# Optimization experiments

Measured on AMD Instinct MI355X. Metric: run time of the kernel, lower is better.

The kernel has to match this reference:

```python
import jax, jax.numpy as jnp
import numpy as np

B, T, E, K, D = 8, 4096, 1024, 128, 1024


def setup_inputs() -> dict:
    key = jax.random.key(0)
    ks = jax.random.split(key, 5)
    scale_w = 1.0 / np.sqrt(E)
    x = jax.random.normal(ks[0], (B, T, E), dtype=jnp.float32)
    mu = jax.random.normal(ks[1], (1, K, E), dtype=jnp.float32) * scale_w
    bias = jax.random.normal(ks[2], (1, K), dtype=jnp.float32) * scale_w
    Wr = jax.random.normal(ks[3], (D, K * E), dtype=jnp.float32) * (1.0 / np.sqrt(K * E))
    Wl = jax.random.normal(ks[4], (K * E, D), dtype=jnp.float32) * (1.0 / np.sqrt(D))
    k = jnp.float32(1.0)
    b = jnp.float32(0.0)
    return {"x": x, "mu": mu, "bias": bias, "Wr": Wr, "Wl": Wl, "k": k, "b": b}


def reference(x, mu, bias, Wr, Wl, k, b):
    # x: [B,T,E], mu: [1,K,E]
    inv_sqrt_E = 1.0 / jnp.sqrt(jnp.float32(E))
    # att = mu @ x^T / sqrt(E) -> [B,K,T]
    att = jnp.einsum('ke,bte->bkt', mu[0], x) * inv_sqrt_E
    part = jax.nn.logsumexp(att, axis=-1)            # [B,K]
    attp = jax.nn.softmax(att, axis=-1)              # [B,K,T]
    sel = jnp.einsum('bkt,bte->bke', attp, x)        # [B,K,E]
    # lre*sel + (1-lre)*sel is mathematically identity; preserved from source
    lre = jax.nn.sigmoid(part - bias)[:, :, None]
    sel = lre * sel + (1.0 - lre) * sel
    # low-rank MLP (dsel is computed but unused in the original forward)
    xr = jax.nn.relu(sel.reshape(x.shape[0], -1) @ Wr.T)   # [B,D]
    dsel = (xr @ Wl.T).reshape(sel.shape)                   # [B,K,E] (unused)
    # attention-transpose combine + residual + affine
    dx = jnp.einsum('bkt,bke->bte', attp, sel)              # [B,T,E]
    out = k * (x + dx) + b
    return out
```

## Files before the change

kernel.cpp:

```cpp
#include <hip/hip_runtime.h>

#define B_ 8
#define T_ 4096
#define E_ 1024
#define K_ 128

typedef __bf16 bf16;
typedef bf16 bf16x8 __attribute__((ext_vector_type(8)));
typedef bf16 bf16x4 __attribute__((ext_vector_type(4)));
typedef float f32x4 __attribute__((ext_vector_type(4)));

__global__ __launch_bounds__(256) void k0_cvt_mu(const float* __restrict__ mu,
                                                 bf16* __restrict__ mub) {
    int i = blockIdx.x * 256 + threadIdx.x;
    mub[i] = (bf16)mu[i];
}

__global__ __launch_bounds__(256) void k1_att(const float* __restrict__ x,
                                              const bf16* __restrict__ mub,
                                              bf16* __restrict__ attPh,
                                              bf16* __restrict__ xb) {
    const int b = blockIdx.z;
    const int h = blockIdx.y;
    const int t0 = blockIdx.x * 64;
    const int tid = threadIdx.x;
    const int w = tid >> 6, lane = tid & 63, g = lane >> 4, ln = lane & 15;

    __shared__ bf16 xs[64][72];
    __shared__ bf16 ms[128][72];

    f32x4 acc[8];
#pragma unroll
    for (int m = 0; m < 8; ++m) acc[m] = (f32x4){0.f, 0.f, 0.f, 0.f};

    const int rx = tid >> 4, cx = (tid & 15) * 4;
    const int rm = tid >> 3, cm = (tid & 7) * 8;

    for (int c = 0; c < 8; ++c) {
        const int ebase = h * 512 + c * 64;
#pragma unroll
        for (int p = 0; p < 4; ++p) {
            const int row = p * 16 + rx;
            f32x4 v = *(const f32x4*)(x + ((size_t)(b * T_ + t0 + row)) * E_ + ebase + cx);
            bf16x4 o;
            o[0] = (bf16)v[0]; o[1] = (bf16)v[1]; o[2] = (bf16)v[2]; o[3] = (bf16)v[3];
            *(bf16x4*)&xs[row][cx] = o;
            *(bf16x4*)(xb + ((size_t)(b * T_ + t0 + row)) * E_ + ebase + cx) = o;
        }
#pragma unroll
        for (int p = 0; p < 4; ++p) {
            const int row = p * 32 + rm;
            *(bf16x8*)&ms[row][cm] =
                *(const bf16x8*)(mub + (size_t)row * E_ + ebase + cm);
        }
        __syncthreads();
#pragma unroll
        for (int s = 0; s < 2; ++s) {
            const int es = s * 32 + g * 8;
            bf16x8 bf = *(const bf16x8*)&xs[w * 16 + ln][es];
#pragma unroll
            for (int m = 0; m < 8; ++m) {
                bf16x8 af = *(const bf16x8*)&ms[m * 16 + ln][es];
                acc[m] = __builtin_amdgcn_mfma_f32_16x16x32_bf16(af, bf, acc[m], 0, 0, 0);
            }
        }
        __syncthreads();
    }
    const int t = t0 + w * 16 + ln;
#pragma unroll
    for (int m = 0; m < 8; ++m)
#pragma unroll
        for (int r = 0; r < 4; ++r)
            attPh[(((size_t)h * B_ + b) * K_ + m * 16 + g * 4 + r) * T_ + t] =
                (bf16)acc[m][r];
}

__global__ __launch_bounds__(256) void k2_softmax(const bf16* __restrict__ attPh,
                                                  bf16* __restrict__ attp) {
    const int row = blockIdx.x;
    const int tid = threadIdx.x;
    const bf16* p0 = attPh + (size_t)row * T_;
    const bf16* p1 = attPh + (size_t)(B_ * K_) * T_ + (size_t)row * T_;
    float v[16];
    float m = -1e30f;
#pragma unroll
    for (int i = 0; i < 2; ++i) {
        const int off = (i * 256 + tid) * 8;
        bf16x8 a = *(const bf16x8*)(p0 + off);
        bf16x8 c = *(const bf16x8*)(p1 + off);
#pragma unroll
        for (int j = 0; j < 8; ++j) {
            const float val = ((float)a[j] + (float)c[j]) * 0.03125f;
            v[i * 8 + j] = val;
            m = fmaxf(m, val);
        }
    }
#pragma unroll
    for (int off = 32; off > 0; off >>= 1) m = fmaxf(m, __shfl_xor(m, off));
    __shared__ float redm[4], reds[4];
    const int wave = tid >> 6, lane = tid & 63;
    if (lane == 0) redm[wave] = m;
    __syncthreads();
    m = fmaxf(fmaxf(redm[0], redm[1]), fmaxf(redm[2], redm[3]));
    float s = 0.f;
#pragma unroll
    for (int i = 0; i < 16; ++i) {
        v[i] = __expf(v[i] - m);
        s += v[i];
    }
#pragma unroll
    for (int off = 32; off > 0; off >>= 1) s += __shfl_xor(s, off);
    if (lane == 0) reds[wave] = s;
    __syncthreads();
    const float inv = 1.f / (reds[0] + reds[1] + reds[2] + reds[3]);
#pragma unroll
    for (int i = 0; i < 2; ++i) {
        const int off = (i * 256 + tid) * 8;
        bf16x8 o;
#pragma unroll
        for (int j = 0; j < 8; ++j) o[j] = (bf16)(v[i * 8 + j] * inv);
        *(bf16x8*)(attp + (size_t)row * T_ + off) = o;
    }
}

__global__ __launch_bounds__(256) void k4_sel(const bf16* __restrict__ xb,
                                              const bf16* __restrict__ attp,
                                              bf16* __restrict__ selpT) {
    const int e0 = blockIdx.x * 64;
    const int chunk = blockIdx.y;
    const int b = blockIdx.z;
    const int tid = threadIdx.x;
    const int w = tid >> 6, lane = tid & 63, g = lane >> 4, ln = lane & 15;

    __shared__ __align__(16) char smem[27648];
    bf16 (*as_)[72] = (bf16(*)[72])smem;
    bf16 (*xs2)[72] = (bf16(*)[72])(smem + 18432);

    f32x4 acc[8];
#pragma unroll
    for (int m = 0; m < 8; ++m) acc[m] = (f32x4){0.f, 0.f, 0.f, 0.f};

    const int rs = tid >> 3, cs = (tid & 7) * 8;

    for (int sub = 0; sub < 8; ++sub) {
        const int tc = chunk * 512 + sub * 64;
#pragma unroll
        for (int p = 0; p < 4; ++p) {
            const int row = p * 32 + rs;
            *(bf16x8*)&as_[row][cs] =
                *(const bf16x8*)(attp + ((size_t)(b * K_ + row)) * T_ + tc + cs);
        }
#pragma unroll
        for (int p = 0; p < 2; ++p) {
            const int row = p * 32 + rs;
            *(bf16x8*)&xs2[row][cs] =
                *(const bf16x8*)(xb + ((size_t)(b * T_ + tc + row)) * E_ + e0 + cs);
        }
        __syncthreads();
#pragma unroll
        for (int s = 0; s < 2; ++s) {
            const int ts = s * 32 + g * 8;
            bf16x8 bf;
#pragma unroll
            for (int j = 0; j < 8; ++j) bf[j] = xs2[ts + j][w * 16 + ln];
#pragma unroll
            for (int m = 0; m < 8; ++m) {
                bf16x8 af = *(const bf16x8*)&as_[m * 16 + ln][ts];
                acc[m] = __builtin_amdgcn_mfma_f32_16x16x32_bf16(af, bf, acc[m], 0, 0, 0);
            }
        }
        __syncthreads();
    }
    bf16 (*tlb)[136] = (bf16(*)[136])smem;
#pragma unroll
    for (int m = 0; m < 8; ++m)
#pragma unroll
        for (int r = 0; r < 4; ++r)
            tlb[w * 16 + ln][m * 16 + g * 4 + r] = (bf16)acc[m][r];
    __syncthreads();
    bf16* dst = selpT + ((size_t)chunk * B_ + b) * E_ * K_ + (size_t)e0 * K_;
#pragma unroll
    for (int rr = 0; rr < 4; ++rr) {
        const int slot = rr * 256 + tid;
        const int ee = slot >> 4;
        const int kq = slot & 15;
        bf16x8 o = *(bf16x8*)&tlb[ee][kq * 8];
        *(bf16x8*)(dst + (size_t)ee * K_ + kq * 8) = o;
    }
}

__global__ __launch_bounds__(256) void k4b_reduce(const bf16* __restrict__ selpT,
                                                  bf16* __restrict__ selbT) {
    const size_t gid = (size_t)blockIdx.x * 256 + threadIdx.x;
    const size_t f = gid * 8;
    float s[8];
#pragma unroll
    for (int j = 0; j < 8; ++j) s[j] = 0.f;
#pragma unroll
    for (int c = 0; c < 8; ++c) {
        bf16x8 v = *(const bf16x8*)(selpT + (size_t)c * (B_ * E_ * K_) + f);
#pragma unroll
        for (int j = 0; j < 8; ++j) s[j] += (float)v[j];
    }
    bf16x8 o;
#pragma unroll
    for (int j = 0; j < 8; ++j) o[j] = (bf16)s[j];
    *(bf16x8*)(selbT + f) = o;
}

__global__ __launch_bounds__(256) void k5_out(const bf16* __restrict__ xb,
                                              const bf16* __restrict__ attp,
                                              const bf16* __restrict__ selbT,
                                              const float* __restrict__ kp,
                                              const float* __restrict__ bp,
                                              float* __restrict__ out) {
    const int b = blockIdx.z;
    const int t0 = blockIdx.x * 64;
    const int e0 = blockIdx.y * 64;
    const int tid = threadIdx.x;
    const int w = tid >> 6, lane = tid & 63, g = lane >> 4, ln = lane & 15;
    const float kk = kp[0], bb = bp[0];
    __shared__ bf16 pT[64][128];
    __shared__ bf16 sb[64][136];

    {
        const int u = tid & 3;
        const int kr = tid >> 2;
#pragma unroll
        for (int p = 0; p < 2; ++p) {
            const int k = p * 64 + kr;
            const bf16* src = attp + ((size_t)b * K_ + k) * T_ + t0 + u * 16;
#pragma unroll
            for (int hh = 0; hh < 2; ++hh) {
                bf16x8 v = *(const bf16x8*)(src + hh * 8);
#pragma unroll
                for (int j = 0; j < 8; ++j) {
                    const int t = u * 16 + hh * 8 + j;
                    pT[t][k ^ (j << 3)] = v[j];
                }
            }
        }
    }
    {
        const int er = tid >> 2;
        const int kc = (tid & 3) * 32;
        const bf16* src = selbT + ((size_t)b * E_ + e0 + er) * K_ + kc;
#pragma unroll
        for (int q = 0; q < 4; ++q)
            *(bf16x8*)&sb[er][kc + q * 8] = *(const bf16x8*)(src + q * 8);
    }
    __syncthreads();

    const int tl = w * 16 + ln;
    f32x4 acc[4];
#pragma unroll
    for (int m = 0; m < 4; ++m) acc[m] = (f32x4){0.f, 0.f, 0.f, 0.f};

#pragma unroll
    for (int ks = 0; ks < 4; ++ks) {
        const int k0 = ks * 32 + g * 8;
        bf16x8 bfr = *(const bf16x8*)&pT[tl][k0 ^ ((tl & 7) << 3)];
#pragma unroll
        for (int m = 0; m < 4; ++m) {
            bf16x8 af = *(const bf16x8*)&sb[m * 16 + ln][k0];
            acc[m] = __builtin_amdgcn_mfma_f32_16x16x32_bf16(af, bfr, acc[m], 0, 0, 0);
        }
    }

    const int t = t0 + tl;
#pragma unroll
    for (int m = 0; m < 4; ++m) {
        const int e = e0 + m * 16 + g * 4;
        const size_t idx = ((size_t)b * T_ + t) * E_ + e;
        bf16x4 xv = *(const bf16x4*)(xb + idx);
        f32x4 o;
        o[0] = kk * ((float)xv[0] + acc[m][0]) + bb;
        o[1] = kk * ((float)xv[1] + acc[m][1]) + bb;
        o[2] = kk * ((float)xv[2] + acc[m][2]) + bb;
        o[3] = kk * ((float)xv[3] + acc[m][3]) + bb;
        *(f32x4*)(out + idx) = o;
    }
}

extern "C" void kernel_launch(void* const* d_in, const int* in_sizes, int n_in,
                              void* d_out, int out_size, void* d_ws, size_t ws_size,
                              hipStream_t stream) {
    const float* x  = (const float*)d_in[0];
    const float* mu = (const float*)d_in[1];
    const float* kp = (const float*)d_in[5];
    const float* bp = (const float*)d_in[6];
    float* out = (float*)d_out;

    char* ws = (char*)d_ws;
    bf16*  attPh = (bf16*)(ws);
    bf16*  selpT = (bf16*)(ws);
    bf16*  attp  = (bf16*)(ws + 16777216);
    bf16*  selbT = (bf16*)(ws + 25165824);
    bf16*  mub   = (bf16*)(ws + 27262976);
    bf16*  xb    = (bf16*)(ws + 27525120);

    k0_cvt_mu<<<dim3(512), 256, 0, stream>>>(mu, mub);
    k1_att<<<dim3(64, 2, 8), 256, 0, stream>>>(x, mub, attPh, xb);
    k2_softmax<<<dim3(1024), 256, 0, stream>>>(attPh, attp);
    k4_sel<<<dim3(16, 8, 8), 256, 0, stream>>>(xb, attp, selpT);
    k4b_reduce<<<dim3(512), 256, 0, stream>>>(selpT, selbT);
    k5_out<<<dim3(64, 16, 8), 256, 0, stream>>>(xb, attp, selbT, kp, bp, out);
}
```

Baseline: 135.1 us.

## Pre-transpose attention probabilities and read MFMA operands directly from global

```diff
diff --git a/kernel.cpp b/kernel.cpp
--- a/kernel.cpp
+++ b/kernel.cpp
@@ -123,6 +123,28 @@
     }
 }
 
+__global__ __launch_bounds__(256) void k3_transpose(const bf16* __restrict__ attp,
+                                                    bf16* __restrict__ attpT) {
+    const int b = blockIdx.y;
+    const int t0 = blockIdx.x * 64;
+    const int tid = threadIdx.x;
+    __shared__ bf16 tile[128][66];
+    const int kk = tid >> 1, half = tid & 1;
+#pragma unroll
+    for (int q = 0; q < 4; ++q)
+        *(bf16x8*)&tile[kk][half * 32 + q * 8] =
+            *(const bf16x8*)(attp + ((size_t)b * K_ + kk) * T_ + t0 + half * 32 + q * 8);
+    __syncthreads();
+    const int tt = tid & 63, kslot = (tid >> 6) * 32;
+#pragma unroll
+    for (int q = 0; q < 4; ++q) {
+        bf16x8 o;
+#pragma unroll
+        for (int j = 0; j < 8; ++j) o[j] = tile[kslot + q * 8 + j][tt];
+        *(bf16x8*)(attpT + ((size_t)b * T_ + t0 + tt) * K_ + kslot + q * 8) = o;
+    }
+}
+
 __global__ __launch_bounds__(256) void k4_sel(const bf16* __restrict__ xb,
                                               const bf16* __restrict__ attp,
                                               bf16* __restrict__ selpT) {
@@ -209,7 +231,7 @@
 }
 
 __global__ __launch_bounds__(256) void k5_out(const bf16* __restrict__ xb,
-                                              const bf16* __restrict__ attp,
+                                              const bf16* __restrict__ attpT,
                                               const bf16* __restrict__ selbT,
                                               const float* __restrict__ kp,
                                               const float* __restrict__ bp,
@@ -220,49 +242,21 @@
     const int tid = threadIdx.x;
     const int w = tid >> 6, lane = tid & 63, g = lane >> 4, ln = lane & 15;
     const float kk = kp[0], bb = bp[0];
-    __shared__ bf16 pT[64][128];
-    __shared__ bf16 sb[64][136];
-
-    {
-        const int u = tid & 3;
-        const int kr = tid >> 2;
-#pragma unroll
-        for (int p = 0; p < 2; ++p) {
-            const int k = p * 64 + kr;
-            const bf16* src = attp + ((size_t)b * K_ + k) * T_ + t0 + u * 16;
-#pragma unroll
-            for (int hh = 0; hh < 2; ++hh) {
-                bf16x8 v = *(const bf16x8*)(src + hh * 8);
-#pragma unroll
-                for (int j = 0; j < 8; ++j) {
-                    const int t = u * 16 + hh * 8 + j;
-                    pT[t][k ^ (j << 3)] = v[j];
-                }
-            }
-        }
-    }
-    {
-        const int er = tid >> 2;
-        const int kc = (tid & 3) * 32;
-        const bf16* src = selbT + ((size_t)b * E_ + e0 + er) * K_ + kc;
-#pragma unroll
-        for (int q = 0; q < 4; ++q)
-            *(bf16x8*)&sb[er][kc + q * 8] = *(const bf16x8*)(src + q * 8);
-    }
-    __syncthreads();
 
     const int tl = w * 16 + ln;
     f32x4 acc[4];
 #pragma unroll
     for (int m = 0; m < 4; ++m) acc[m] = (f32x4){0.f, 0.f, 0.f, 0.f};
 
+    const bf16* brow = attpT + ((size_t)b * T_ + t0 + tl) * K_;
+    const bf16* arow = selbT + ((size_t)b * E_ + e0 + ln) * K_;
 #pragma unroll
     for (int ks = 0; ks < 4; ++ks) {
         const int k0 = ks * 32 + g * 8;
-        bf16x8 bfr = *(const bf16x8*)&pT[tl][k0 ^ ((tl & 7) << 3)];
+        bf16x8 bfr = *(const bf16x8*)(brow + k0);
 #pragma unroll
         for (int m = 0; m < 4; ++m) {
-            bf16x8 af = *(const bf16x8*)&sb[m * 16 + ln][k0];
+            bf16x8 af = *(const bf16x8*)(arow + (size_t)(m * 16) * K_ + k0);
             acc[m] = __builtin_amdgcn_mfma_f32_16x16x32_bf16(af, bfr, acc[m], 0, 0, 0);
         }
     }
@@ -298,11 +292,13 @@
     bf16*  selbT = (bf16*)(ws + 25165824);
     bf16*  mub   = (bf16*)(ws + 27262976);
     bf16*  xb    = (bf16*)(ws + 27525120);
+    bf16*  attpT = (bf16*)(ws + 94633984);
 
     k0_cvt_mu<<<dim3(512), 256, 0, stream>>>(mu, mub);
     k1_att<<<dim3(64, 2, 8), 256, 0, stream>>>(x, mub, attPh, xb);
     k2_softmax<<<dim3(1024), 256, 0, stream>>>(attPh, attp);
+    k3_transpose<<<dim3(64, 8), 256, 0, stream>>>(attp, attpT);
     k4_sel<<<dim3(16, 8, 8), 256, 0, stream>>>(xb, attp, selpT);
     k4b_reduce<<<dim3(512), 256, 0, stream>>>(selpT, selbT);
-    k5_out<<<dim3(64, 16, 8), 256, 0, stream>>>(xb, attp, selbT, kp, bp, out);
-}
+    k5_out<<<dim3(64, 16, 8), 256, 0, stream>>>(xb, attpT, selbT, kp, bp, out);
+}
```

Measured after the change: 186.5 us. +38.1%, slower.
